# Kernel tuning notes

Hardware: AMD Instinct MI355X
Metric: run time of the kernel (lower is better)

The kernel has to match this reference:

```python
import jax, jax.numpy as jnp
import numpy as np

E = 8        # num_experts
TOPK = 2     # num_experts_per_tok
D = 1024     # n_embd
H = 2816     # grok FFN hidden dim (multiple_of-rounded 2/3*4*D)
B, T = 4, 2048
COEFF = 0.01 # moe_aux_loss_coeff


def setup_inputs() -> dict:
    key = jax.random.key(0)
    ks = jax.random.split(key, 8)
    s = 0.02  # weight scale so activations stay well-conditioned
    return {
        "x": jax.random.normal(ks[0], (B, T, D), jnp.float32),
        "gate_w": jax.random.normal(ks[1], (D, E), jnp.float32) * s,
        "expert_gate": jax.random.normal(ks[2], (E, D, H), jnp.float32) * s,
        "expert_up": jax.random.normal(ks[3], (E, D, H), jnp.float32) * s,
        "expert_down": jax.random.normal(ks[4], (E, H, D), jnp.float32) * s,
        "shared_gate": jax.random.normal(ks[5], (D, H), jnp.float32) * s,
        "shared_up": jax.random.normal(ks[6], (D, H), jnp.float32) * s,
        "shared_down": jax.random.normal(ks[7], (H, D), jnp.float32) * s,
    }


def _grok_ffn(x, g, u, d):
    # down(gelu(gate(x)) * up(x)); torch F.gelu default = exact erf gelu
    return (jax.nn.gelu(x @ g, approximate=False) * (x @ u)) @ d


def reference(x, gate_w, expert_gate, expert_up, expert_down,
              shared_gate, shared_up, shared_down):
    Bb, Tt, Dd = x.shape
    N = Bb * Tt
    xf = x.reshape(N, Dd)

    # --- router ---
    logits = (xf @ gate_w).astype(jnp.float32)            # (N, E)
    top_logits, top_idx = jax.lax.top_k(logits, TOPK)     # (N, K)
    top_w = jax.nn.softmax(top_logits, axis=-1)           # (N, K)
    gates = jax.nn.softmax(logits, axis=-1)               # (N, E)
    f = jnp.mean(jax.nn.one_hot(top_idx[:, 0], E, dtype=jnp.float32), axis=0)
    P = gates.mean(axis=0)
    aux_loss = COEFF * E * jnp.sum(f * P)

    # dense combine weights (N, E): 0 for unassigned experts
    comb = jnp.zeros((N, E), xf.dtype).at[
        jnp.arange(N)[:, None], top_idx].add(top_w.astype(xf.dtype))

    # --- experts: loop over small fixed E, weight-masked dense FFN ---
    out = jnp.zeros_like(xf)
    for e in range(E):
        ye = _grok_ffn(xf, expert_gate[e], expert_up[e], expert_down[e])
        out = out + comb[:, e:e + 1] * ye

    out = out.reshape(Bb, Tt, Dd)
    out = out + _grok_ffn(xf, shared_gate, shared_up, shared_down).reshape(Bb, Tt, Dd)
    return out, aux_loss
```

## Files before the change

### kernel.cpp

```cpp
#include <hip/hip_runtime.h>
#include <hip/hip_bf16.h>

#define NTOK 8192
#define DIM  1024
#define HID  2816
#define NI   (2 * HID)
#define ROWS_CAP 26880
#define TC256 104
#define TC128 208

typedef __bf16 bf16x8 __attribute__((ext_vector_type(8)));
typedef float  f32x4  __attribute__((ext_vector_type(4)));

__device__ __forceinline__ unsigned short f2bf(float f) {
  unsigned int x = __float_as_uint(f);
  unsigned int r = (x + 0x7fffu + ((x >> 16) & 1u)) >> 16;
  return (unsigned short)r;
}
__device__ __forceinline__ float gelu_erf(float g) {
  return 0.5f * g * (1.0f + erff(g * 0.70710678118654752f));
}

__device__ __forceinline__ void gload16(const void* g, void* l) {
  __builtin_amdgcn_global_load_lds(
      (__attribute__((address_space(1))) void*)(g),
      (__attribute__((address_space(3))) void*)(l), 16, 0, 0);
}

__device__ __forceinline__ void transpose64(const float* __restrict__ in,
                                            unsigned short* __restrict__ out,
                                            int R, int C, int iloff) {
  __shared__ float t[64][65];
  int c0 = blockIdx.x * 64, r0 = blockIdx.y * 64;
  int tid = threadIdx.x;
  int lr = tid >> 4;
  int lc4 = (tid & 15) * 4;
  #pragma unroll
  for (int it = 0; it < 4; ++it) {
    int row = lr + it * 16;
    float4 v = *(const float4*)(in + (size_t)(r0 + row) * C + c0 + lc4);
    t[row][lc4] = v.x; t[row][lc4 + 1] = v.y;
    t[row][lc4 + 2] = v.z; t[row][lc4 + 3] = v.w;
  }
  __syncthreads();
  #pragma unroll
  for (int it = 0; it < 4; ++it) {
    int cloc = lr + it * 16;
    int c = c0 + cloc;
    int rowil = (iloff < 0) ? c : (((c >> 4) << 5) + (c & 15) + iloff);
    ushort4 w = make_ushort4(f2bf(t[lc4][cloc]), f2bf(t[lc4 + 1][cloc]),
                             f2bf(t[lc4 + 2][cloc]), f2bf(t[lc4 + 3][cloc]));
    *(ushort4*)(out + (size_t)rowil * R + r0 + lc4) = w;
  }
}

__global__ __launch_bounds__(256) void k_transpose_DH(
    const float* __restrict__ eg, const float* __restrict__ eu,
    const float* __restrict__ sg, const float* __restrict__ su,
    unsigned short* __restrict__ WI, unsigned short* __restrict__ SI) {
  int z = blockIdx.z;
  const float* in; unsigned short* out; int off;
  if (z < 8)        { in = eg + (size_t)z * DIM * HID;       out = WI + (size_t)z * NI * DIM; off = 0; }
  else if (z < 16)  { in = eu + (size_t)(z - 8) * DIM * HID; out = WI + (size_t)(z - 8) * NI * DIM; off = 16; }
  else if (z == 16) { in = sg; out = SI; off = 0; }
  else              { in = su; out = SI; off = 16; }
  transpose64(in, out, DIM, HID, off);
}

__global__ __launch_bounds__(256) void k_transpose_HD(
    const float* __restrict__ ed, const float* __restrict__ sd,
    unsigned short* __restrict__ WdT, unsigned short* __restrict__ SdT) {
  int z = blockIdx.z;
  const float* in; unsigned short* out;
  if (z < 8) { in = ed + (size_t)z * HID * DIM; out = WdT + (size_t)z * HID * DIM; }
  else       { in = sd; out = SdT; }
  transpose64(in, out, HID, DIM, -1);
}


__global__ __launch_bounds__(256) void k_router(const float* __restrict__ x,
                                                const float* __restrict__ gw,
                                                unsigned short* __restrict__ xb,
                                                int* __restrict__ top_idx,
                                                float* __restrict__ top_w,
                                                int* __restrict__ counts,
                                                float* __restrict__ f_cnt,
                                                float* __restrict__ P_sum) {
  __shared__ float s_p[8];
  __shared__ int   s_cnt[8];
  __shared__ int   s_f[8];
  int tid = threadIdx.x;
  if (tid < 8) { s_p[tid] = 0.f; s_cnt[tid] = 0; s_f[tid] = 0; }
  __syncthreads();

  int lane = tid & 63, wv = tid >> 6;
  float ploc[8] = {0,0,0,0,0,0,0,0};
  int   cloc[8] = {0,0,0,0,0,0,0,0};
  int   floc[8] = {0,0,0,0,0,0,0,0};

  for (int t = blockIdx.x * 4 + wv; t < NTOK; t += 2048) {
    const float4* xr = (const float4*)(x + (size_t)t * DIM) + lane * 4;
    float4 v0 = xr[0], v1 = xr[1], v2 = xr[2], v3 = xr[3];
    float xv[16] = {v0.x, v0.y, v0.z, v0.w, v1.x, v1.y, v1.z, v1.w,
                    v2.x, v2.y, v2.z, v2.w, v3.x, v3.y, v3.z, v3.w};
    ushort4* xw = (ushort4*)(xb + (size_t)t * DIM + lane * 16);
    #pragma unroll
    for (int q = 0; q < 4; ++q)
      xw[q] = make_ushort4(f2bf(xv[q * 4]), f2bf(xv[q * 4 + 1]),
                           f2bf(xv[q * 4 + 2]), f2bf(xv[q * 4 + 3]));
    float acc[8] = {0.f,0.f,0.f,0.f,0.f,0.f,0.f,0.f};
    #pragma unroll
    for (int i = 0; i < 16; ++i) {
      const float* g = gw + (size_t)(lane * 16 + i) * 8;
      #pragma unroll
      for (int e = 0; e < 8; ++e) acc[e] += xv[i] * g[e];
    }
    #pragma unroll
    for (int e = 0; e < 8; ++e) {
      #pragma unroll
      for (int off = 32; off > 0; off >>= 1)
        acc[e] += __shfl_xor(acc[e], off, 64);
    }
    if (lane == 0) {
      int i1 = 0; float l1 = acc[0];
      #pragma unroll
      for (int e = 1; e < 8; ++e) if (acc[e] > l1) { l1 = acc[e]; i1 = e; }
      int i2 = -1; float l2 = -3.0e38f;
      #pragma unroll
      for (int e = 0; e < 8; ++e) if (e != i1 && acc[e] > l2) { l2 = acc[e]; i2 = e; }
      float e2 = expf(l2 - l1);
      float inv12 = 1.0f / (1.0f + e2);
      top_idx[2 * t] = i1; top_idx[2 * t + 1] = i2;
      top_w[2 * t] = inv12; top_w[2 * t + 1] = e2 * inv12;
      float s = 0.f, p[8];
      #pragma unroll
      for (int e = 0; e < 8; ++e) { p[e] = expf(acc[e] - l1); s += p[e]; }
      float invs = 1.0f / s;
      #pragma unroll
      for (int e = 0; e < 8; ++e) {
        ploc[e] += p[e] * invs;
        cloc[e] += (e == i1) + (e == i2);
        floc[e] += (e == i1);
      }
    }
  }
  if (lane == 0) {
    #pragma unroll
    for (int e = 0; e < 8; ++e) {
      atomicAdd(&s_p[e], ploc[e]);
      atomicAdd(&s_cnt[e], cloc[e]);
      atomicAdd(&s_f[e], floc[e]);
    }
  }
  __syncthreads();
  if (tid < 8) {
    atomicAdd(&P_sum[tid], s_p[tid]);
    atomicAdd(&counts[tid], s_cnt[tid]);
    atomicAdd(&f_cnt[tid], (float)s_f[tid]);
  }
}


__global__ __launch_bounds__(256) void k_setup(const int* __restrict__ counts,
                                               int* __restrict__ cursors,
                                               int* __restrict__ te256,
                                               int* __restrict__ te128,
                                               int* __restrict__ perm,
                                               float* __restrict__ wrow) {
  int t = threadIdx.x;
  for (int r = t; r < ROWS_CAP; r += 256) {
    perm[r] = (r < NTOK) ? r : 0;
    wrow[r] = (r < NTOK) ? 1.0f : 0.0f;
  }
  if (t == 0) {
    int so[8], pe[8];
    int cur = NTOK;
    for (int e = 0; e < 8; ++e) {
      so[e] = cur;
      pe[e] = ((counts[e] + 255) >> 8) << 8;
      cur += pe[e];
    }
    for (int e = 0; e < 8; ++e) cursors[e] = so[e];
    for (int T = 0; T < TC256; ++T) {
      int r0 = T << 8;
      int ex;
      if (T < NTOK / 256) ex = 8;
      else if (r0 < cur) {
        ex = 0;
        for (int e = 0; e < 8; ++e) if (r0 >= so[e] && r0 < so[e] + pe[e]) ex = e;
      } else ex = -1;
      te256[T] = ex;
    }
    for (int ht = 0; ht < TC128; ++ht) {
      int r0 = ht << 7;
      int ex;
      if (ht < NTOK / 128) ex = 8;
      else if (r0 < cur) {
        ex = 0;
        for (int e = 0; e < 8; ++e) if (r0 >= so[e] && r0 < so[e] + pe[e]) ex = e;
      } else ex = -1;
      te128[ht] = ex;
    }
  }
}

__global__ __launch_bounds__(256) void k_scatter(const int* __restrict__ top_idx,
                                                 const float* __restrict__ top_w,
                                                 int* __restrict__ cursors,
                                                 int* __restrict__ perm,
                                                 float* __restrict__ wrow) {
  int i = blockIdx.x * 256 + threadIdx.x;
  if (i < NTOK * 2) {
    int e = top_idx[i];
    float w = top_w[i];
    int slot = atomicAdd(&cursors[e], 1);
    perm[slot] = i >> 1;
    wrow[slot] = w;
  }
}


__global__ __launch_bounds__(512) void k_stageA(const unsigned short* __restrict__ xb,
    const unsigned short* __restrict__ WI, const unsigned short* __restrict__ SI,
    const int* __restrict__ perm, const int* __restrict__ te256,
    unsigned short* __restrict__ h, int T0, int row_base) {
  int T = T0 + blockIdx.y;
  int e = te256[T];
  if (e < 0) return;
  const unsigned short* B = (e < 8) ? WI + (size_t)e * NI * DIM : SI;
  int rows0 = T * 256;
  int c0i = blockIdx.x * 256;

  __shared__ unsigned short As[2][256 * 64];
  __shared__ unsigned short Bs[2][256 * 64];

  int tid = threadIdx.x, lane = tid & 63, w = tid >> 6;
  int wr = w >> 2, wc = w & 3;
  int rlo = lane >> 3;
  int koff = ((lane & 7) ^ rlo) * 8;
  int fr = lane & 15;

  int prow[4];
  #pragma unroll
  for (int i = 0; i < 4; ++i) prow[i] = perm[rows0 + i * 64 + w * 8 + rlo];
  const unsigned short* bsrc[4];
  #pragma unroll
  for (int i = 0; i < 4; ++i)
    bsrc[i] = B + (size_t)(c0i + i * 64 + w * 8 + rlo) * DIM + koff;

  f32x4 acc[8][4] = {};

  auto stage = [&](int b, int k0) {
    #pragma unroll
    for (int i = 0; i < 4; ++i)
      gload16(xb + (size_t)prow[i] * DIM + k0 + koff, (char*)As[b] + (i * 64 + w * 8) * 128);
    #pragma unroll
    for (int i = 0; i < 4; ++i)
      gload16(bsrc[i] + k0, (char*)Bs[b] + (i * 64 + w * 8) * 128);
  };

  auto compute = [&](int b) {
    #pragma unroll
    for (int kk = 0; kk < 2; ++kk) {
      int kbyte = (kk * 64 + (lane >> 4) * 16) ^ ((lane & 7) << 4);
      bf16x8 a[8], bf[4];
      #pragma unroll
      for (int mi = 0; mi < 8; ++mi)
        a[mi] = *(const bf16x8*)((const char*)As[b] + (wr * 128 + mi * 16 + fr) * 128 + kbyte);
      #pragma unroll
      for (int ni = 0; ni < 4; ++ni)
        bf[ni] = *(const bf16x8*)((const char*)Bs[b] + (wc * 64 + ni * 16 + fr) * 128 + kbyte);
      #pragma unroll
      for (int mi = 0; mi < 8; ++mi) {
        #pragma unroll
        for (int ni = 0; ni < 4; ++ni)
          acc[mi][ni] = __builtin_amdgcn_mfma_f32_16x16x32_bf16(a[mi], bf[ni], acc[mi][ni], 0, 0, 0);
      }
    }
  };

  stage(0, 0);
  int cur = 0;
  for (int kb = 0; kb < DIM / 64 - 1; ++kb) {
    stage(cur ^ 1, (kb + 1) * 64);
    __builtin_amdgcn_sched_barrier(0);
    asm volatile("s_waitcnt vmcnt(8)" ::: "memory");
    __builtin_amdgcn_s_barrier();
    __builtin_amdgcn_sched_barrier(0);
    __builtin_amdgcn_s_setprio(1);
    compute(cur);
    __builtin_amdgcn_s_setprio(0);
    __builtin_amdgcn_s_barrier();
    cur ^= 1;
  }
  asm volatile("s_waitcnt vmcnt(0)" ::: "memory");
  __builtin_amdgcn_s_barrier();
  __builtin_amdgcn_sched_barrier(0);
  compute(cur);

  #pragma unroll
  for (int mi = 0; mi < 8; ++mi) {
    #pragma unroll
    for (int p = 0; p < 2; ++p) {
      #pragma unroll
      for (int j = 0; j < 4; ++j) {
        int rg = rows0 - row_base + wr * 128 + mi * 16 + (lane >> 4) * 4 + j;
        int cg = blockIdx.x * 128 + wc * 32 + p * 16 + fr;
        float g = acc[mi][2 * p][j];
        float u = acc[mi][2 * p + 1][j];
        h[(size_t)rg * HID + cg] = f2bf(gelu_erf(g) * u);
      }
    }
  }
}


template <bool STORE>
__global__ __launch_bounds__(256) void k_stageB(const unsigned short* __restrict__ h,
    const unsigned short* __restrict__ WdT, const unsigned short* __restrict__ SdT,
    const int* __restrict__ perm, const float* __restrict__ wrow,
    const int* __restrict__ te128,
    float* __restrict__ out, int t0, int row_base) {
  int tile = t0 + blockIdx.y;
  int e = te128[tile];
  if (e < 0) return;
  const unsigned short* Bd = (e < 8) ? WdT + (size_t)e * DIM * HID : SdT;
  int rows0 = tile * 128;
  int n0 = blockIdx.x * 128;

  __shared__ unsigned short As[2][128 * 64];
  __shared__ unsigned short Bs[2][128 * 64];

  int tid = threadIdx.x, lane = tid & 63, wv = tid >> 6;
  int wr = wv >> 1, wc = wv & 1;
  int rlo = lane >> 3;
  int koff = (((lane & 7) ^ rlo) * 8);
  int rsw = (lane & 7) << 4;

  f32x4 acc[4][4] = {};

  auto stage = [&](int b, int k0) {
    #pragma unroll
    for (int i = 0; i < 4; ++i) {
      int rb = i * 32 + wv * 8;
      int r = rb + rlo;
      gload16(h + (size_t)(rows0 - row_base + r) * HID + k0 + koff, (char*)As[b] + rb * 128);
      gload16(Bd + (size_t)(n0 + r) * HID + k0 + koff, (char*)Bs[b] + rb * 128);
    }
  };

  auto compute = [&](int b) {
    #pragma unroll
    for (int kk = 0; kk < 2; ++kk) {
      int kbyte = (kk * 64 + (lane >> 4) * 16) ^ rsw;
      bf16x8 a[4], bb[4];
      #pragma unroll
      for (int mi = 0; mi < 4; ++mi)
        a[mi] = *(const bf16x8*)((const char*)As[b] + (wr * 64 + mi * 16 + (lane & 15)) * 128 + kbyte);
      #pragma unroll
      for (int ni = 0; ni < 4; ++ni)
        bb[ni] = *(const bf16x8*)((const char*)Bs[b] + (wc * 64 + ni * 16 + (lane & 15)) * 128 + kbyte);
      #pragma unroll
      for (int mi = 0; mi < 4; ++mi) {
        #pragma unroll
        for (int ni = 0; ni < 4; ++ni)
          acc[mi][ni] = __builtin_amdgcn_mfma_f32_16x16x32_bf16(a[mi], bb[ni], acc[mi][ni], 0, 0, 0);
      }
    }
  };

  stage(0, 0);
  int cur = 0;
  for (int kb = 0; kb < HID / 64 - 1; ++kb) {
    stage(cur ^ 1, (kb + 1) * 64);
    __builtin_amdgcn_sched_barrier(0);
    asm volatile("s_waitcnt vmcnt(8)" ::: "memory");
    __builtin_amdgcn_s_barrier();
    __builtin_amdgcn_sched_barrier(0);
    __builtin_amdgcn_s_setprio(1);
    compute(cur);
    __builtin_amdgcn_s_setprio(0);
    __builtin_amdgcn_s_barrier();
    cur ^= 1;
  }
  asm volatile("s_waitcnt vmcnt(0)" ::: "memory");
  __builtin_amdgcn_s_barrier();
  __builtin_amdgcn_sched_barrier(0);
  compute(cur);

  #pragma unroll
  for (int mi = 0; mi < 4; ++mi) {
    #pragma unroll
    for (int j = 0; j < 4; ++j) {
      int rl = wr * 64 + mi * 16 + (lane >> 4) * 4 + j;
      int token = perm[rows0 + rl];
      float w = wrow[rows0 + rl];
      #pragma unroll
      for (int ni = 0; ni < 4; ++ni) {
        int col = n0 + wc * 64 + ni * 16 + (lane & 15);
        if (STORE) out[(size_t)token * DIM + col] = w * acc[mi][ni][j];
        else atomicAdd(&out[(size_t)token * DIM + col], w * acc[mi][ni][j]);
      }
    }
  }
}


__global__ void k_aux(const float* __restrict__ f_cnt, const float* __restrict__ P_sum,
                      float* __restrict__ aux_out) {
  if (threadIdx.x == 0 && blockIdx.x == 0) {
    float a = 0.f;
    #pragma unroll
    for (int e = 0; e < 8; ++e) a += f_cnt[e] * P_sum[e];
    a *= 0.01f * 8.f / ((float)NTOK * (float)NTOK);
    aux_out[0] = a;
  }
}


extern "C" void kernel_launch(void* const* d_in, const int* in_sizes, int n_in,
                              void* d_out, int out_size, void* d_ws, size_t ws_size,
                              hipStream_t stream) {
  const float* x  = (const float*)d_in[0];
  const float* gw = (const float*)d_in[1];
  const float* eg = (const float*)d_in[2];
  const float* eu = (const float*)d_in[3];
  const float* ed = (const float*)d_in[4];
  const float* sg = (const float*)d_in[5];
  const float* su = (const float*)d_in[6];
  const float* sd = (const float*)d_in[7];
  float* out = (float*)d_out;

  char* ws = (char*)d_ws;
  size_t off = 0;
  auto take = [&](size_t sz) { size_t o = off; off += (sz + 255) & ~(size_t)255; return o; };
  const size_t OFF_XB   = take((size_t)NTOK * DIM * 2);
  const size_t OFF_WI   = take((size_t)8 * NI * DIM * 2);
  const size_t OFF_SI   = take((size_t)NI * DIM * 2);
  const size_t OFF_WDT  = take((size_t)8 * HID * DIM * 2);
  const size_t OFF_SDT  = take((size_t)HID * DIM * 2);
  const size_t OFF_TI   = take((size_t)NTOK * 2 * 4);
  const size_t OFF_TW   = take((size_t)NTOK * 2 * 4);
  const size_t OFF_PERM = take((size_t)ROWS_CAP * 4);
  const size_t OFF_WROW = take((size_t)ROWS_CAP * 4);
  const size_t OFF_STATS= take(256);
  const size_t OFF_CURS = take(256);
  const size_t OFF_TE2  = take(TC256 * 4);
  const size_t OFF_TE1  = take(TC128 * 4);
  const size_t OFF_H    = off;

  const size_t TILE_H_BYTES = (size_t)256 * HID * 2;
  size_t avail = (ws_size > OFF_H) ? (ws_size - OFF_H) : 0;
  int G = (int)((avail / TILE_H_BYTES < (size_t)TC256) ? (avail / TILE_H_BYTES) : (size_t)TC256);
  if (G < 1) return;

  unsigned short* xb  = (unsigned short*)(ws + OFF_XB);
  unsigned short* WI  = (unsigned short*)(ws + OFF_WI);
  unsigned short* SI  = (unsigned short*)(ws + OFF_SI);
  unsigned short* WdT = (unsigned short*)(ws + OFF_WDT);
  unsigned short* SdT = (unsigned short*)(ws + OFF_SDT);
  int* top_idx        = (int*)(ws + OFF_TI);
  float* top_w        = (float*)(ws + OFF_TW);
  int* perm           = (int*)(ws + OFF_PERM);
  float* wrow         = (float*)(ws + OFF_WROW);
  int* counts         = (int*)(ws + OFF_STATS);
  float* f_cnt        = (float*)(ws + OFF_STATS + 32);
  float* P_sum        = (float*)(ws + OFF_STATS + 64);
  int* cursors        = (int*)(ws + OFF_CURS);
  int* te256          = (int*)(ws + OFF_TE2);
  int* te128          = (int*)(ws + OFF_TE1);
  unsigned short* hbuf = (unsigned short*)(ws + OFF_H);

  hipMemsetAsync(ws + OFF_STATS, 0, 256, stream);

  k_transpose_DH<<<dim3(HID / 64, DIM / 64, 18), 256, 0, stream>>>(
      eg, eu, sg, su, WI, SI);
  k_transpose_HD<<<dim3(DIM / 64, HID / 64, 9), 256, 0, stream>>>(
      ed, sd, WdT, SdT);

  k_router<<<512, 256, 0, stream>>>(x, gw, xb, top_idx, top_w, counts, f_cnt, P_sum);
  k_setup<<<1, 256, 0, stream>>>(counts, cursors, te256, te128, perm, wrow);
  k_scatter<<<NTOK * 2 / 256, 256, 0, stream>>>(top_idx, top_w, cursors, perm, wrow);

  for (int T0 = 0; T0 < TC256; T0 += G) {
    int nt = (TC256 - T0 < G) ? (TC256 - T0) : G;
    int row_base = T0 * 256;
    k_stageA<<<dim3(NI / 256, nt), 512, 0, stream>>>(xb, WI, SI, perm, te256,
                                                     hbuf, T0, row_base);
    int h0t = T0 * 2, hn = nt * 2;
    int ns = 0;
    if (h0t < 64) { ns = 64 - h0t; if (ns > hn) ns = hn; }
    int ne = hn - ns;
    if (ns > 0)
      k_stageB<true><<<dim3(DIM / 128, ns), 256, 0, stream>>>(hbuf, WdT, SdT, perm, wrow,
                                                              te128, out, h0t, row_base);
    if (ne > 0)
      k_stageB<false><<<dim3(DIM / 128, ne), 256, 0, stream>>>(hbuf, WdT, SdT, perm, wrow,
                                                               te128, out, h0t + ns, row_base);
  }

  k_aux<<<1, 64, 0, stream>>>(f_cnt, P_sum, out + (size_t)NTOK * DIM);
}
```

Before: 925.2 us.

## Interleave global prefetch with MFMA sub-phases in gate/up GEMM main loop

Restructures the K-loop of the gate/up expert GEMM into four sub-phases per k-block. Each sub-phase loads a slice of A fragments from LDS, issues a quarter of the next tile's global-to-LDS loads, and runs its MFMAs between workgroup barriers. The goal is to spread memory traffic across the compute phase and overlap LDS reads with MFMA work, in the style of hipBLASLt ping-pong schedules. The cost is many more s_barrier calls per k-block, a full vmcnt(0) wait at the end of each block, and reduced freedom for the compiler to schedule.

```diff
diff --git a/kernel.cpp b/kernel.cpp
--- a/kernel.cpp
+++ b/kernel.cpp
@@ -239,6 +239,8 @@
   int rlo = lane >> 3;
   int koff = ((lane & 7) ^ rlo) * 8;
   int fr = lane & 15;
+  int kby0 = ((lane >> 4) * 16) ^ ((lane & 7) << 4);
+  int kby1 = (64 + (lane >> 4) * 16) ^ ((lane & 7) << 4);
 
   int prow[4];
   #pragma unroll
@@ -250,53 +252,81 @@
 
   f32x4 acc[8][4] = {};
 
-  auto stage = [&](int b, int k0) {
-    #pragma unroll
-    for (int i = 0; i < 4; ++i)
-      gload16(xb + (size_t)prow[i] * DIM + k0 + koff, (char*)As[b] + (i * 64 + w * 8) * 128);
-    #pragma unroll
-    for (int i = 0; i < 4; ++i)
-      gload16(bsrc[i] + k0, (char*)Bs[b] + (i * 64 + w * 8) * 128);
-  };
-
-  auto compute = [&](int b) {
-    #pragma unroll
-    for (int kk = 0; kk < 2; ++kk) {
-      int kbyte = (kk * 64 + (lane >> 4) * 16) ^ ((lane & 7) << 4);
-      bf16x8 a[8], bf[4];
-      #pragma unroll
-      for (int mi = 0; mi < 8; ++mi)
-        a[mi] = *(const bf16x8*)((const char*)As[b] + (wr * 128 + mi * 16 + fr) * 128 + kbyte);
-      #pragma unroll
-      for (int ni = 0; ni < 4; ++ni)
-        bf[ni] = *(const bf16x8*)((const char*)Bs[b] + (wc * 64 + ni * 16 + fr) * 128 + kbyte);
-      #pragma unroll
-      for (int mi = 0; mi < 8; ++mi) {
-        #pragma unroll
-        for (int ni = 0; ni < 4; ++ni)
-          acc[mi][ni] = __builtin_amdgcn_mfma_f32_16x16x32_bf16(a[mi], bf[ni], acc[mi][ni], 0, 0, 0);
-      }
-    }
-  };
-
-  stage(0, 0);
-  int cur = 0;
-  for (int kb = 0; kb < DIM / 64 - 1; ++kb) {
-    stage(cur ^ 1, (kb + 1) * 64);
-    __builtin_amdgcn_sched_barrier(0);
-    asm volatile("s_waitcnt vmcnt(8)" ::: "memory");
-    __builtin_amdgcn_s_barrier();
-    __builtin_amdgcn_sched_barrier(0);
-    __builtin_amdgcn_s_setprio(1);
-    compute(cur);
-    __builtin_amdgcn_s_setprio(0);
-    __builtin_amdgcn_s_barrier();
-    cur ^= 1;
-  }
+  #pragma unroll
+  for (int i = 0; i < 4; ++i)
+    gload16(xb + (size_t)prow[i] * DIM + koff, (char*)As[0] + (i * 64 + w * 8) * 128);
+  #pragma unroll
+  for (int i = 0; i < 4; ++i)
+    gload16(bsrc[i], (char*)Bs[0] + (i * 64 + w * 8) * 128);
   asm volatile("s_waitcnt vmcnt(0)" ::: "memory");
   __builtin_amdgcn_s_barrier();
   __builtin_amdgcn_sched_barrier(0);
-  compute(cur);
+
+  int cur = 0;
+  for (int kb = 0; kb < DIM / 64; ++kb) {
+    const char* Ab = (const char*)As[cur];
+    const char* Bb = (const char*)Bs[cur];
+    char* An = (char*)As[cur ^ 1];
+    char* Bn = (char*)Bs[cur ^ 1];
+    int k1 = (kb + 1) * 64;
+    bool pf = (kb < DIM / 64 - 1);
+    bf16x8 bfr[4][2];
+
+    #pragma unroll
+    for (int q = 0; q < 4; ++q) {
+      bf16x8 a[2][2];
+      #pragma unroll
+      for (int m = 0; m < 2; ++m) {
+        const char* ar = Ab + (wr * 128 + (2 * q + m) * 16 + fr) * 128;
+        a[m][0] = *(const bf16x8*)(ar + kby0);
+        a[m][1] = *(const bf16x8*)(ar + kby1);
+      }
+      if (q == 0) {
+        #pragma unroll
+        for (int ni = 0; ni < 4; ++ni) {
+          const char* br = Bb + (wc * 64 + ni * 16 + fr) * 128;
+          bfr[ni][0] = *(const bf16x8*)(br + kby0);
+          bfr[ni][1] = *(const bf16x8*)(br + kby1);
+        }
+      }
+      if (pf) {
+        if (q == 0) {
+          gload16(xb + (size_t)prow[0] * DIM + k1 + koff, An + (0 * 64 + w * 8) * 128);
+          gload16(xb + (size_t)prow[1] * DIM + k1 + koff, An + (1 * 64 + w * 8) * 128);
+        } else if (q == 1) {
+          gload16(xb + (size_t)prow[2] * DIM + k1 + koff, An + (2 * 64 + w * 8) * 128);
+          gload16(xb + (size_t)prow[3] * DIM + k1 + koff, An + (3 * 64 + w * 8) * 128);
+        } else if (q == 2) {
+          gload16(bsrc[0] + k1, Bn + (0 * 64 + w * 8) * 128);
+          gload16(bsrc[1] + k1, Bn + (1 * 64 + w * 8) * 128);
+        } else {
+          gload16(bsrc[2] + k1, Bn + (2 * 64 + w * 8) * 128);
+          gload16(bsrc[3] + k1, Bn + (3 * 64 + w * 8) * 128);
+        }
+      }
+      __builtin_amdgcn_s_barrier();
+      __builtin_amdgcn_s_setprio(1);
+      #pragma unroll
+      for (int kk = 0; kk < 2; ++kk) {
+        #pragma unroll
+        for (int m = 0; m < 2; ++m) {
+          #pragma unroll
+          for (int ni = 0; ni < 4; ++ni)
+            acc[2 * q + m][ni] = __builtin_amdgcn_mfma_f32_16x16x32_bf16(
+                a[m][kk], bfr[ni][kk], acc[2 * q + m][ni], 0, 0, 0);
+        }
+      }
+      __builtin_amdgcn_s_setprio(0);
+      if (q < 3) {
+        __builtin_amdgcn_s_barrier();
+      } else {
+        asm volatile("s_waitcnt vmcnt(0)" ::: "memory");
+        __builtin_amdgcn_s_barrier();
+        __builtin_amdgcn_sched_barrier(0);
+      }
+    }
+    cur ^= 1;
+  }
 
   #pragma unroll
   for (int mi = 0; mi < 8; ++mi) {
```

Measured after the change: 908.3 us. Within noise of the previous version (-1.8%).
